# Kernel tuning notes

Measured on AMD Instinct MI355X. Metric: run time of the kernel, lower is better.

The kernel has to match this reference:

```python
import jax, jax.numpy as jnp
import numpy as np
from jax import lax

N_BANDS, TAPS, CUTOFF, BETA = 4, 62, 0.15, 9.0
B, T = 16, 262144


def make_pqmf_filters(N=N_BANDS, taps=TAPS, cutoff=CUTOFF, beta=BETA):
    # scipy.signal.firwin(taps+1, cutoff, window=('kaiser', beta)) reimplemented:
    numtaps = taps + 1
    m = np.arange(numtaps) - (numtaps - 1) / 2.0
    qmf = cutoff * np.sinc(cutoff * m) * np.kaiser(numtaps, beta)
    qmf /= qmf.sum()  # unit DC gain (firwin scale=True, lowpass)
    k = np.arange(N)[:, None]
    n = np.arange(numtaps)[None, :]
    const = (2 * k + 1) * (np.pi / (2 * N)) * (n - (taps - 1) / 2.0)
    phase = ((-1.0) ** np.arange(N))[:, None] * np.pi / 4.0
    H = 2.0 * qmf * np.cos(const + phase)
    G = 2.0 * qmf * np.cos(const - phase)
    return H.astype(np.float32), G.astype(np.float32)


def setup_inputs() -> dict:
    key = jax.random.key(0)
    x = jax.random.normal(key, (B, 1, T), dtype=jnp.float32)
    H, G = make_pqmf_filters()
    return {"x": x, "H": jnp.asarray(H), "G": jnp.asarray(G)}


def reference(x, H, G):
    # Round trip: synthesis(analysis(x)). x: (B,1,T); H,G: (N, taps+1).
    N = H.shape[0]
    pad = (H.shape[1] - 1) // 2  # taps//2 = 31
    dn = ('NCH', 'OIH', 'NCH')
    # analysis: stride-1 FIR bank then the updown_filter strided conv, which is
    # exactly take-every-Nth-sample (updown_filter[0,k,k]=1).
    sub = lax.conv_general_dilated(x, H[:, None, :], (1,), [(pad, pad)],
                                   dimension_numbers=dn)  # (B, N, T)
    sub = sub[:, :, ::N]  # (B, N, T//N)
    # synthesis: conv1d_transpose(updown_filter*N, stride N) == zero-stuff upsample
    # scaled by N; fused here via lhs_dilation. Extra N-1 right pad matches the
    # trailing zeros of the TF transpose-conv output (length T//N * N).
    recon = lax.conv_general_dilated(sub * N, G[None, :, :], (1,),
                                     [(pad, pad + N - 1)], lhs_dilation=(N,),
                                     dimension_numbers=dn)  # (B, 1, T)
    return recon
```

## Files before the change

### kernel.cpp

```cpp
#include <hip/hip_runtime.h>

#define TT 262144
#define BB 16
#define SS 65536
#define QPB 1024
#define TILEQ 1056
#define PX(j) ((j) + ((j) >> 2))
#define LDSQ 1320

__global__ __launch_bounds__(256) void prep_w(const float* __restrict__ H,
                                              const float* __restrict__ G,
                                              float* __restrict__ W) {
    int t = blockIdx.x * 256 + threadIdx.x;
    int e = t >> 2;
    int k = t & 3;
    bool valid = (e < 4 * 132);
    float acc = 0.f;
    if (valid) {
        int p = e / 132;
        int i = e % 132;
        int dd = 126 + p - i;
        if (dd >= 0 && dd <= 124) {
            int j0 = (3 - p) & 3;
#pragma unroll
            for (int jj = 0; jj < 16; ++jj) {
                int j = j0 + 4 * jj;
                if (j <= 62) {
                    int a = 124 - j - dd;
                    if (a >= 0 && a <= 62) acc += H[k * 63 + a] * G[k * 63 + j];
                }
            }
        }
    }
    acc += __shfl_xor(acc, 1);
    acc += __shfl_xor(acc, 2);
    if (valid && k == 0) W[e] = 4.0f * acc;
}

__global__ __launch_bounds__(256) void pqmf_fused(const float* __restrict__ x,
                                                  const float* __restrict__ Wg,
                                                  const float* __restrict__ H,
                                                  const float* __restrict__ G,
                                                  float* __restrict__ out) {
    __shared__ float4 xs4[LDSQ];

    const int tid = threadIdx.x;
    const int b = blockIdx.y;
    const int Q0 = blockIdx.x * QPB;
    const float4* X4 = reinterpret_cast<const float4*>(x + (size_t)b * TT);

    const int gq0 = Q0 - 16;
#pragma unroll
    for (int it = 0; it < 5; ++it) {
        int j = tid + it * 256;
        if (j < TILEQ) {
            int gq = gq0 + j;
            xs4[PX(j)] = (gq >= 0 && gq < SS) ? X4[gq]
                                              : make_float4(0.f, 0.f, 0.f, 0.f);
        }
    }
    __syncthreads();

    const float4* xp = xs4 + 5 * tid;

    float4 a0 = make_float4(0.f, 0.f, 0.f, 0.f);
    float4 a1 = a0, a2 = a0, a3 = a0;

    const float4* W4 = reinterpret_cast<const float4*>(Wg);

#define TAP(k, x0, x1, x2, x3)                                                 \
    {                                                                          \
        const float4 W0 = W4[(k)];                          \
        const float4 W1 = W4[33 + (k)];                     \
        const float4 W2 = W4[66 + (k)];                     \
        const float4 W3 = W4[99 + (k)];                     \
        a0.x = fmaf(W0.w, (x0).w, fmaf(W0.z, (x0).z, fmaf(W0.y, (x0).y, fmaf(W0.x, (x0).x, a0.x)))); \
        a0.y = fmaf(W1.w, (x0).w, fmaf(W1.z, (x0).z, fmaf(W1.y, (x0).y, fmaf(W1.x, (x0).x, a0.y)))); \
        a0.z = fmaf(W2.w, (x0).w, fmaf(W2.z, (x0).z, fmaf(W2.y, (x0).y, fmaf(W2.x, (x0).x, a0.z)))); \
        a0.w = fmaf(W3.w, (x0).w, fmaf(W3.z, (x0).z, fmaf(W3.y, (x0).y, fmaf(W3.x, (x0).x, a0.w)))); \
        a1.x = fmaf(W0.w, (x1).w, fmaf(W0.z, (x1).z, fmaf(W0.y, (x1).y, fmaf(W0.x, (x1).x, a1.x)))); \
        a1.y = fmaf(W1.w, (x1).w, fmaf(W1.z, (x1).z, fmaf(W1.y, (x1).y, fmaf(W1.x, (x1).x, a1.y)))); \
        a1.z = fmaf(W2.w, (x1).w, fmaf(W2.z, (x1).z, fmaf(W2.y, (x1).y, fmaf(W2.x, (x1).x, a1.z)))); \
        a1.w = fmaf(W3.w, (x1).w, fmaf(W3.z, (x1).z, fmaf(W3.y, (x1).y, fmaf(W3.x, (x1).x, a1.w)))); \
        a2.x = fmaf(W0.w, (x2).w, fmaf(W0.z, (x2).z, fmaf(W0.y, (x2).y, fmaf(W0.x, (x2).x, a2.x)))); \
        a2.y = fmaf(W1.w, (x2).w, fmaf(W1.z, (x2).z, fmaf(W1.y, (x2).y, fmaf(W1.x, (x2).x, a2.y)))); \
        a2.z = fmaf(W2.w, (x2).w, fmaf(W2.z, (x2).z, fmaf(W2.y, (x2).y, fmaf(W2.x, (x2).x, a2.z)))); \
        a2.w = fmaf(W3.w, (x2).w, fmaf(W3.z, (x2).z, fmaf(W3.y, (x2).y, fmaf(W3.x, (x2).x, a2.w)))); \
        a3.x = fmaf(W0.w, (x3).w, fmaf(W0.z, (x3).z, fmaf(W0.y, (x3).y, fmaf(W0.x, (x3).x, a3.x)))); \
        a3.y = fmaf(W1.w, (x3).w, fmaf(W1.z, (x3).z, fmaf(W1.y, (x3).y, fmaf(W1.x, (x3).x, a3.y)))); \
        a3.z = fmaf(W2.w, (x3).w, fmaf(W2.z, (x3).z, fmaf(W2.y, (x3).y, fmaf(W2.x, (x3).x, a3.z)))); \
        a3.w = fmaf(W3.w, (x3).w, fmaf(W3.z, (x3).z, fmaf(W3.y, (x3).y, fmaf(W3.x, (x3).x, a3.w)))); \
    }

    float4 w0 = xp[0], w1 = xp[1], w2 = xp[2], w3 = xp[3];

#pragma unroll 1
    for (int mm = 0; mm < 8; ++mm) {
        const float4* xq = xp + 5 * mm;
        const int k0 = 4 * mm;
        float4 n0 = xq[5];
        float4 n1 = xq[6];
        float4 n2 = xq[7];
        float4 n3 = xq[8];
        TAP(k0 + 0, w0, w1, w2, w3)
        TAP(k0 + 1, w1, w2, w3, n0)
        TAP(k0 + 2, w2, w3, n0, n1)
        TAP(k0 + 3, w3, n0, n1, n2)
        w0 = n0; w1 = n1; w2 = n2; w3 = n3;
    }
    TAP(32, w0, w1, w2, w3)
#undef TAP

    float4* ob4 = reinterpret_cast<float4*>(out + (size_t)b * TT);
    const int t0 = tid * 4;
    const int u0 = Q0 + t0;
    if ((unsigned)(u0 - 16) < (unsigned)(SS - 32))     ob4[u0]     = a0;
    if ((unsigned)(u0 + 1 - 16) < (unsigned)(SS - 32)) ob4[u0 + 1] = a1;
    if ((unsigned)(u0 + 2 - 16) < (unsigned)(SS - 32)) ob4[u0 + 2] = a2;
    if ((unsigned)(u0 + 3 - 16) < (unsigned)(SS - 32)) ob4[u0 + 3] = a3;

    const bool edgeLo = (blockIdx.x == 0);
    const bool edgeHi = (blockIdx.x == gridDim.x - 1);
    if (edgeLo || edgeHi) {
        const int q_local = tid >> 4;
        const int s_idx = tid & 15;
        const int u = edgeLo ? q_local : (SS - 16 + q_local);
        const int s = u - 7 + s_idx;
        float c0 = 0.f, c1 = 0.f, c2 = 0.f, c3 = 0.f;
        if (s >= 0 && s < SS) {
            const float* xsf = reinterpret_cast<const float*>(xs4);
            const int lbase = 4 * s - 31 - 4 * Q0 + 64;
            float s0 = 0.f, s1 = 0.f, s2 = 0.f, s3 = 0.f;
#pragma unroll
            for (int a = 0; a < 63; ++a) {
                int ef = lbase + a;
                float xv = xsf[ef + 4 * (ef >> 4)];
                s0 += xv * H[a];
                s1 += xv * H[63 + a];
                s2 += xv * H[126 + a];
                s3 += xv * H[189 + a];
            }
            const int d4 = 4 * (s - u);
            {
                int j = d4 + 31;
                if (j <= 62) c0 = s0 * G[j] + s1 * G[63 + j] + s2 * G[126 + j] + s3 * G[189 + j];
            }
            {
                int j = d4 + 30;
                c1 = s0 * G[j] + s1 * G[63 + j] + s2 * G[126 + j] + s3 * G[189 + j];
            }
            {
                int j = d4 + 29;
                c2 = s0 * G[j] + s1 * G[63 + j] + s2 * G[126 + j] + s3 * G[189 + j];
            }
            {
                int j = d4 + 28;
                c3 = s0 * G[j] + s1 * G[63 + j] + s2 * G[126 + j] + s3 * G[189 + j];
            }
        }
#pragma unroll
        for (int m = 8; m >= 1; m >>= 1) {
            c0 += __shfl_xor(c0, m);
            c1 += __shfl_xor(c1, m);
            c2 += __shfl_xor(c2, m);
            c3 += __shfl_xor(c3, m);
        }
        if (s_idx == 0) {
            float4 v = make_float4(4.f * c0, 4.f * c1, 4.f * c2, 4.f * c3);
            ob4[u] = v;
        }
    }
}

extern "C" void kernel_launch(void* const* d_in, const int* in_sizes, int n_in,
                              void* d_out, int out_size, void* d_ws, size_t ws_size,
                              hipStream_t stream) {
    const float* x = (const float*)d_in[0];
    const float* H = (const float*)d_in[1];
    const float* G = (const float*)d_in[2];
    float* outp = (float*)d_out;
    float* W = (float*)d_ws;

    hipLaunchKernelGGL(prep_w, dim3(9), dim3(256), 0, stream, H, G, W);
    hipLaunchKernelGGL(pqmf_fused, dim3(SS / QPB, BB), dim3(256), 0, stream,
                       x, W, H, G, outp);
}
```

Before: 27.45 us.

## Batch weight loads as 16-wide vectors, unguard interior tile loads, spread edge fixups

Each loop iteration now fetches the weights for four taps as 64-byte vector loads instead of sixteen separate float4 loads. Interior blocks load their input tile with no bounds checks, issuing all global loads before any LDS stores. The 32 edge output quads, previously computed by the two edge blocks with 256 threads, now go one per block to 32 different blocks, using 16 threads that read x straight from global memory. The aim is fewer scalar/vector load instructions on the hot path and less serial tail work in the two edge blocks, at the cost of more registers and a small uncoalesced global read in 32 blocks.

```diff
diff --git a/kernel.cpp b/kernel.cpp
--- a/kernel.cpp
+++ b/kernel.cpp
@@ -7,6 +7,8 @@
 #define TILEQ 1056
 #define PX(j) ((j) + ((j) >> 2))
 #define LDSQ 1320
+
+typedef float floatx16 __attribute__((ext_vector_type(16), aligned(16)));
 
 __global__ __launch_bounds__(256) void prep_w(const float* __restrict__ H,
                                               const float* __restrict__ G,
@@ -45,20 +47,33 @@
     __shared__ float4 xs4[LDSQ];
 
     const int tid = threadIdx.x;
+    const int bx = blockIdx.x;
     const int b = blockIdx.y;
-    const int Q0 = blockIdx.x * QPB;
+    const int Q0 = bx * QPB;
     const float4* X4 = reinterpret_cast<const float4*>(x + (size_t)b * TT);
 
     const int gq0 = Q0 - 16;
-#pragma unroll
-    for (int it = 0; it < 5; ++it) {
-        int j = tid + it * 256;
-        if (j < TILEQ) {
-            int gq = gq0 + j;
-            xs4[PX(j)] = (gq >= 0 && gq < SS) ? X4[gq]
-                                              : make_float4(0.f, 0.f, 0.f, 0.f);
-        }
-    }
+    float4 r0, r1, r2, r3, r4;
+    if (bx > 0 && bx < 63) {
+        r0 = X4[gq0 + tid];
+        r1 = X4[gq0 + tid + 256];
+        r2 = X4[gq0 + tid + 512];
+        r3 = X4[gq0 + tid + 768];
+        if (tid < 32) r4 = X4[gq0 + tid + 1024];
+    } else {
+        const float4 z = make_float4(0.f, 0.f, 0.f, 0.f);
+        int g0 = gq0 + tid, g1 = g0 + 256, g2 = g0 + 512, g3 = g0 + 768, g4 = g0 + 1024;
+        r0 = ((unsigned)g0 < (unsigned)SS) ? X4[g0] : z;
+        r1 = ((unsigned)g1 < (unsigned)SS) ? X4[g1] : z;
+        r2 = ((unsigned)g2 < (unsigned)SS) ? X4[g2] : z;
+        r3 = ((unsigned)g3 < (unsigned)SS) ? X4[g3] : z;
+        if (tid < 32) r4 = ((unsigned)g4 < (unsigned)SS) ? X4[g4] : z;
+    }
+    xs4[PX(tid)]       = r0;
+    xs4[PX(tid + 256)] = r1;
+    xs4[PX(tid + 512)] = r2;
+    xs4[PX(tid + 768)] = r3;
+    if (tid < 32) xs4[PX(tid + 1024)] = r4;
     __syncthreads();
 
     const float4* xp = xs4 + 5 * tid;
@@ -66,50 +81,64 @@
     float4 a0 = make_float4(0.f, 0.f, 0.f, 0.f);
     float4 a1 = a0, a2 = a0, a3 = a0;
 
-    const float4* W4 = reinterpret_cast<const float4*>(Wg);
-
-#define TAP(k, x0, x1, x2, x3)                                                 \
+#define TAPX(d, x0, x1, x2, x3)                                                \
     {                                                                          \
-        const float4 W0 = W4[(k)];                          \
-        const float4 W1 = W4[33 + (k)];                     \
-        const float4 W2 = W4[66 + (k)];                     \
-        const float4 W3 = W4[99 + (k)];                     \
-        a0.x = fmaf(W0.w, (x0).w, fmaf(W0.z, (x0).z, fmaf(W0.y, (x0).y, fmaf(W0.x, (x0).x, a0.x)))); \
-        a0.y = fmaf(W1.w, (x0).w, fmaf(W1.z, (x0).z, fmaf(W1.y, (x0).y, fmaf(W1.x, (x0).x, a0.y)))); \
-        a0.z = fmaf(W2.w, (x0).w, fmaf(W2.z, (x0).z, fmaf(W2.y, (x0).y, fmaf(W2.x, (x0).x, a0.z)))); \
-        a0.w = fmaf(W3.w, (x0).w, fmaf(W3.z, (x0).z, fmaf(W3.y, (x0).y, fmaf(W3.x, (x0).x, a0.w)))); \
-        a1.x = fmaf(W0.w, (x1).w, fmaf(W0.z, (x1).z, fmaf(W0.y, (x1).y, fmaf(W0.x, (x1).x, a1.x)))); \
-        a1.y = fmaf(W1.w, (x1).w, fmaf(W1.z, (x1).z, fmaf(W1.y, (x1).y, fmaf(W1.x, (x1).x, a1.y)))); \
-        a1.z = fmaf(W2.w, (x1).w, fmaf(W2.z, (x1).z, fmaf(W2.y, (x1).y, fmaf(W2.x, (x1).x, a1.z)))); \
-        a1.w = fmaf(W3.w, (x1).w, fmaf(W3.z, (x1).z, fmaf(W3.y, (x1).y, fmaf(W3.x, (x1).x, a1.w)))); \
-        a2.x = fmaf(W0.w, (x2).w, fmaf(W0.z, (x2).z, fmaf(W0.y, (x2).y, fmaf(W0.x, (x2).x, a2.x)))); \
-        a2.y = fmaf(W1.w, (x2).w, fmaf(W1.z, (x2).z, fmaf(W1.y, (x2).y, fmaf(W1.x, (x2).x, a2.y)))); \
-        a2.z = fmaf(W2.w, (x2).w, fmaf(W2.z, (x2).z, fmaf(W2.y, (x2).y, fmaf(W2.x, (x2).x, a2.z)))); \
-        a2.w = fmaf(W3.w, (x2).w, fmaf(W3.z, (x2).z, fmaf(W3.y, (x2).y, fmaf(W3.x, (x2).x, a2.w)))); \
-        a3.x = fmaf(W0.w, (x3).w, fmaf(W0.z, (x3).z, fmaf(W0.y, (x3).y, fmaf(W0.x, (x3).x, a3.x)))); \
-        a3.y = fmaf(W1.w, (x3).w, fmaf(W1.z, (x3).z, fmaf(W1.y, (x3).y, fmaf(W1.x, (x3).x, a3.y)))); \
-        a3.z = fmaf(W2.w, (x3).w, fmaf(W2.z, (x3).z, fmaf(W2.y, (x3).y, fmaf(W2.x, (x3).x, a3.z)))); \
-        a3.w = fmaf(W3.w, (x3).w, fmaf(W3.z, (x3).z, fmaf(W3.y, (x3).y, fmaf(W3.x, (x3).x, a3.w)))); \
+        a0.x = fmaf(P0[4*(d)+3], (x0).w, fmaf(P0[4*(d)+2], (x0).z, fmaf(P0[4*(d)+1], (x0).y, fmaf(P0[4*(d)+0], (x0).x, a0.x)))); \
+        a0.y = fmaf(P1[4*(d)+3], (x0).w, fmaf(P1[4*(d)+2], (x0).z, fmaf(P1[4*(d)+1], (x0).y, fmaf(P1[4*(d)+0], (x0).x, a0.y)))); \
+        a0.z = fmaf(P2[4*(d)+3], (x0).w, fmaf(P2[4*(d)+2], (x0).z, fmaf(P2[4*(d)+1], (x0).y, fmaf(P2[4*(d)+0], (x0).x, a0.z)))); \
+        a0.w = fmaf(P3[4*(d)+3], (x0).w, fmaf(P3[4*(d)+2], (x0).z, fmaf(P3[4*(d)+1], (x0).y, fmaf(P3[4*(d)+0], (x0).x, a0.w)))); \
+        a1.x = fmaf(P0[4*(d)+3], (x1).w, fmaf(P0[4*(d)+2], (x1).z, fmaf(P0[4*(d)+1], (x1).y, fmaf(P0[4*(d)+0], (x1).x, a1.x)))); \
+        a1.y = fmaf(P1[4*(d)+3], (x1).w, fmaf(P1[4*(d)+2], (x1).z, fmaf(P1[4*(d)+1], (x1).y, fmaf(P1[4*(d)+0], (x1).x, a1.y)))); \
+        a1.z = fmaf(P2[4*(d)+3], (x1).w, fmaf(P2[4*(d)+2], (x1).z, fmaf(P2[4*(d)+1], (x1).y, fmaf(P2[4*(d)+0], (x1).x, a1.z)))); \
+        a1.w = fmaf(P3[4*(d)+3], (x1).w, fmaf(P3[4*(d)+2], (x1).z, fmaf(P3[4*(d)+1], (x1).y, fmaf(P3[4*(d)+0], (x1).x, a1.w)))); \
+        a2.x = fmaf(P0[4*(d)+3], (x2).w, fmaf(P0[4*(d)+2], (x2).z, fmaf(P0[4*(d)+1], (x2).y, fmaf(P0[4*(d)+0], (x2).x, a2.x)))); \
+        a2.y = fmaf(P1[4*(d)+3], (x2).w, fmaf(P1[4*(d)+2], (x2).z, fmaf(P1[4*(d)+1], (x2).y, fmaf(P1[4*(d)+0], (x2).x, a2.y)))); \
+        a2.z = fmaf(P2[4*(d)+3], (x2).w, fmaf(P2[4*(d)+2], (x2).z, fmaf(P2[4*(d)+1], (x2).y, fmaf(P2[4*(d)+0], (x2).x, a2.z)))); \
+        a2.w = fmaf(P3[4*(d)+3], (x2).w, fmaf(P3[4*(d)+2], (x2).z, fmaf(P3[4*(d)+1], (x2).y, fmaf(P3[4*(d)+0], (x2).x, a2.w)))); \
+        a3.x = fmaf(P0[4*(d)+3], (x3).w, fmaf(P0[4*(d)+2], (x3).z, fmaf(P0[4*(d)+1], (x3).y, fmaf(P0[4*(d)+0], (x3).x, a3.x)))); \
+        a3.y = fmaf(P1[4*(d)+3], (x3).w, fmaf(P1[4*(d)+2], (x3).z, fmaf(P1[4*(d)+1], (x3).y, fmaf(P1[4*(d)+0], (x3).x, a3.y)))); \
+        a3.z = fmaf(P2[4*(d)+3], (x3).w, fmaf(P2[4*(d)+2], (x3).z, fmaf(P2[4*(d)+1], (x3).y, fmaf(P2[4*(d)+0], (x3).x, a3.z)))); \
+        a3.w = fmaf(P3[4*(d)+3], (x3).w, fmaf(P3[4*(d)+2], (x3).z, fmaf(P3[4*(d)+1], (x3).y, fmaf(P3[4*(d)+0], (x3).x, a3.w)))); \
     }
 
     float4 w0 = xp[0], w1 = xp[1], w2 = xp[2], w3 = xp[3];
 
 #pragma unroll 1
     for (int mm = 0; mm < 8; ++mm) {
+        const int k0 = 4 * mm;
+        const floatx16 P0 = *reinterpret_cast<const floatx16*>(Wg + 4 * k0);
+        const floatx16 P1 = *reinterpret_cast<const floatx16*>(Wg + 132 + 4 * k0);
+        const floatx16 P2 = *reinterpret_cast<const floatx16*>(Wg + 264 + 4 * k0);
+        const floatx16 P3 = *reinterpret_cast<const floatx16*>(Wg + 396 + 4 * k0);
         const float4* xq = xp + 5 * mm;
-        const int k0 = 4 * mm;
         float4 n0 = xq[5];
         float4 n1 = xq[6];
         float4 n2 = xq[7];
         float4 n3 = xq[8];
-        TAP(k0 + 0, w0, w1, w2, w3)
-        TAP(k0 + 1, w1, w2, w3, n0)
-        TAP(k0 + 2, w2, w3, n0, n1)
-        TAP(k0 + 3, w3, n0, n1, n2)
+        TAPX(0, w0, w1, w2, w3)
+        TAPX(1, w1, w2, w3, n0)
+        TAPX(2, w2, w3, n0, n1)
+        TAPX(3, w3, n0, n1, n2)
         w0 = n0; w1 = n1; w2 = n2; w3 = n3;
     }
-    TAP(32, w0, w1, w2, w3)
-#undef TAP
+#undef TAPX
+
+    {
+        const float4 T0 = *reinterpret_cast<const float4*>(Wg + 128);
+        const float4 T1 = *reinterpret_cast<const float4*>(Wg + 132 + 128);
+        const float4 T2 = *reinterpret_cast<const float4*>(Wg + 264 + 128);
+        const float4 T3 = *reinterpret_cast<const float4*>(Wg + 396 + 128);
+#define TT4(ar, xv)                                                            \
+        ar.x = fmaf(T0.w, (xv).w, fmaf(T0.z, (xv).z, fmaf(T0.y, (xv).y, fmaf(T0.x, (xv).x, ar.x)))); \
+        ar.y = fmaf(T1.w, (xv).w, fmaf(T1.z, (xv).z, fmaf(T1.y, (xv).y, fmaf(T1.x, (xv).x, ar.y)))); \
+        ar.z = fmaf(T2.w, (xv).w, fmaf(T2.z, (xv).z, fmaf(T2.y, (xv).y, fmaf(T2.x, (xv).x, ar.z)))); \
+        ar.w = fmaf(T3.w, (xv).w, fmaf(T3.z, (xv).z, fmaf(T3.y, (xv).y, fmaf(T3.x, (xv).x, ar.w))));
+        TT4(a0, w0)
+        TT4(a1, w1)
+        TT4(a2, w2)
+        TT4(a3, w3)
+#undef TT4
+    }
 
     float4* ob4 = reinterpret_cast<float4*>(out + (size_t)b * TT);
     const int t0 = tid * 4;
@@ -119,28 +148,26 @@
     if ((unsigned)(u0 + 2 - 16) < (unsigned)(SS - 32)) ob4[u0 + 2] = a2;
     if ((unsigned)(u0 + 3 - 16) < (unsigned)(SS - 32)) ob4[u0 + 3] = a3;
 
-    const bool edgeLo = (blockIdx.x == 0);
-    const bool edgeHi = (blockIdx.x == gridDim.x - 1);
-    if (edgeLo || edgeHi) {
-        const int q_local = tid >> 4;
-        const int s_idx = tid & 15;
-        const int u = edgeLo ? q_local : (SS - 16 + q_local);
-        const int s = u - 7 + s_idx;
+    int ue = -1;
+    if (bx < 16) ue = bx;
+    else if (bx >= 48) ue = SS - 64 + bx;
+    if (ue >= 0 && tid < 16) {
+        const float* xb = x + (size_t)b * TT;
+        const int s = ue - 7 + tid;
         float c0 = 0.f, c1 = 0.f, c2 = 0.f, c3 = 0.f;
         if (s >= 0 && s < SS) {
-            const float* xsf = reinterpret_cast<const float*>(xs4);
-            const int lbase = 4 * s - 31 - 4 * Q0 + 64;
+            const int xbase = 4 * s - 31;
             float s0 = 0.f, s1 = 0.f, s2 = 0.f, s3 = 0.f;
 #pragma unroll
             for (int a = 0; a < 63; ++a) {
-                int ef = lbase + a;
-                float xv = xsf[ef + 4 * (ef >> 4)];
+                int xi = xbase + a;
+                float xv = (xi >= 0 && xi < TT) ? xb[xi] : 0.f;
                 s0 += xv * H[a];
                 s1 += xv * H[63 + a];
                 s2 += xv * H[126 + a];
                 s3 += xv * H[189 + a];
             }
-            const int d4 = 4 * (s - u);
+            const int d4 = 4 * (s - ue);
             {
                 int j = d4 + 31;
                 if (j <= 62) c0 = s0 * G[j] + s1 * G[63 + j] + s2 * G[126 + j] + s3 * G[189 + j];
@@ -165,9 +192,9 @@
             c2 += __shfl_xor(c2, m);
             c3 += __shfl_xor(c3, m);
         }
-        if (s_idx == 0) {
+        if (tid == 0) {
             float4 v = make_float4(4.f * c0, 4.f * c1, 4.f * c2, 4.f * c3);
-            ob4[u] = v;
+            ob4[ue] = v;
         }
     }
 }
```

New measurement: 34.25 us. +24.8%, slower.

## Process two half-size tiles per block with register-prefetched second tile

Applied to the files above, without the earlier changes.

Blocks shrink to 128 threads and 512 quads per tile, and each block now handles two tiles (bx and bx+64). The second tile's global loads go into registers before the first tile is computed, then get stored to a second LDS buffer. The aim is to hide global load latency behind compute. The grid drops to 64x16 blocks of 128 threads, which lowers parallelism and occupancy across the device. Edge handling is split into two passes of 8 outputs to fit the smaller block.

```diff
diff --git a/kernel.cpp b/kernel.cpp
--- a/kernel.cpp
+++ b/kernel.cpp
@@ -3,10 +3,11 @@
 #define TT 262144
 #define BB 16
 #define SS 65536
-#define QPB 1024
-#define TILEQ 1056
+#define QPB 512
+#define TILEQ 544
+#define NTHR 128
 #define PX(j) ((j) + ((j) >> 2))
-#define LDSQ 1320
+#define LDSQ 680
 
 __global__ __launch_bounds__(256) void prep_w(const float* __restrict__ H,
                                               const float* __restrict__ G,
@@ -36,37 +37,6 @@
     acc += __shfl_xor(acc, 2);
     if (valid && k == 0) W[e] = 4.0f * acc;
 }
-
-__global__ __launch_bounds__(256) void pqmf_fused(const float* __restrict__ x,
-                                                  const float* __restrict__ Wg,
-                                                  const float* __restrict__ H,
-                                                  const float* __restrict__ G,
-                                                  float* __restrict__ out) {
-    __shared__ float4 xs4[LDSQ];
-
-    const int tid = threadIdx.x;
-    const int b = blockIdx.y;
-    const int Q0 = blockIdx.x * QPB;
-    const float4* X4 = reinterpret_cast<const float4*>(x + (size_t)b * TT);
-
-    const int gq0 = Q0 - 16;
-#pragma unroll
-    for (int it = 0; it < 5; ++it) {
-        int j = tid + it * 256;
-        if (j < TILEQ) {
-            int gq = gq0 + j;
-            xs4[PX(j)] = (gq >= 0 && gq < SS) ? X4[gq]
-                                              : make_float4(0.f, 0.f, 0.f, 0.f);
-        }
-    }
-    __syncthreads();
-
-    const float4* xp = xs4 + 5 * tid;
-
-    float4 a0 = make_float4(0.f, 0.f, 0.f, 0.f);
-    float4 a1 = a0, a2 = a0, a3 = a0;
-
-    const float4* W4 = reinterpret_cast<const float4*>(Wg);
 
 #define TAP(k, x0, x1, x2, x3)                                                 \
     {                                                                          \
@@ -92,8 +62,15 @@
         a3.w = fmaf(W3.w, (x3).w, fmaf(W3.z, (x3).z, fmaf(W3.y, (x3).y, fmaf(W3.x, (x3).x, a3.w)))); \
     }
 
+__device__ __forceinline__ void compute_tile(const float4* __restrict__ xsb,
+                                             const float4* __restrict__ W4,
+                                             float4* __restrict__ ob4,
+                                             int Q0, int tid) {
+    const float4* xp = xsb + 5 * tid;
+    float4 a0 = make_float4(0.f, 0.f, 0.f, 0.f);
+    float4 a1 = a0, a2 = a0, a3 = a0;
+
     float4 w0 = xp[0], w1 = xp[1], w2 = xp[2], w3 = xp[3];
-
 #pragma unroll 1
     for (int mm = 0; mm < 8; ++mm) {
         const float4* xq = xp + 5 * mm;
@@ -109,26 +86,27 @@
         w0 = n0; w1 = n1; w2 = n2; w3 = n3;
     }
     TAP(32, w0, w1, w2, w3)
-#undef TAP
-
-    float4* ob4 = reinterpret_cast<float4*>(out + (size_t)b * TT);
-    const int t0 = tid * 4;
-    const int u0 = Q0 + t0;
+
+    const int u0 = Q0 + 4 * tid;
     if ((unsigned)(u0 - 16) < (unsigned)(SS - 32))     ob4[u0]     = a0;
     if ((unsigned)(u0 + 1 - 16) < (unsigned)(SS - 32)) ob4[u0 + 1] = a1;
     if ((unsigned)(u0 + 2 - 16) < (unsigned)(SS - 32)) ob4[u0 + 2] = a2;
     if ((unsigned)(u0 + 3 - 16) < (unsigned)(SS - 32)) ob4[u0 + 3] = a3;
-
-    const bool edgeLo = (blockIdx.x == 0);
-    const bool edgeHi = (blockIdx.x == gridDim.x - 1);
-    if (edgeLo || edgeHi) {
-        const int q_local = tid >> 4;
+}
+
+__device__ __forceinline__ void edge16(const float* __restrict__ xsf, int Q0,
+                                       const float* __restrict__ H,
+                                       const float* __restrict__ G,
+                                       float4* __restrict__ ob4,
+                                       int uBase, int tid) {
+#pragma unroll 1
+    for (int half = 0; half < 2; ++half) {
+        const int q_local = (tid >> 4) + 8 * half;
         const int s_idx = tid & 15;
-        const int u = edgeLo ? q_local : (SS - 16 + q_local);
+        const int u = uBase + q_local;
         const int s = u - 7 + s_idx;
         float c0 = 0.f, c1 = 0.f, c2 = 0.f, c3 = 0.f;
         if (s >= 0 && s < SS) {
-            const float* xsf = reinterpret_cast<const float*>(xs4);
             const int lbase = 4 * s - 31 - 4 * Q0 + 64;
             float s0 = 0.f, s1 = 0.f, s2 = 0.f, s3 = 0.f;
 #pragma unroll
@@ -170,6 +148,65 @@
             ob4[u] = v;
         }
     }
+}
+
+__global__ __launch_bounds__(NTHR) void pqmf_fused(const float* __restrict__ x,
+                                                   const float* __restrict__ Wg,
+                                                   const float* __restrict__ H,
+                                                   const float* __restrict__ G,
+                                                   float* __restrict__ out) {
+    __shared__ float4 xs4[2][LDSQ];
+
+    const int tid = threadIdx.x;
+    const int bx = blockIdx.x;
+    const int b = blockIdx.y;
+    const int Q0a = bx * QPB;
+    const int Q0b = (bx + 64) * QPB;
+    const float4* X4 = reinterpret_cast<const float4*>(x + (size_t)b * TT);
+    const float4* W4 = reinterpret_cast<const float4*>(Wg);
+    float4* ob4 = reinterpret_cast<float4*>(out + (size_t)b * TT);
+    const float4 z = make_float4(0.f, 0.f, 0.f, 0.f);
+
+    {
+        const int gq0 = Q0a - 16;
+#pragma unroll
+        for (int it = 0; it < 5; ++it) {
+            int j = tid + it * NTHR;
+            if (j < TILEQ) {
+                int gq = gq0 + j;
+                xs4[0][PX(j)] = ((unsigned)gq < (unsigned)SS) ? X4[gq] : z;
+            }
+        }
+    }
+    __syncthreads();
+
+    const int gq0b = Q0b - 16;
+    float4 r0, r1, r2, r3, r4;
+    {
+        int g0 = gq0b + tid;
+        int g1 = g0 + NTHR, g2 = g0 + 2 * NTHR, g3 = g0 + 3 * NTHR, g4 = g0 + 4 * NTHR;
+        r0 = ((unsigned)g0 < (unsigned)SS) ? X4[g0] : z;
+        r1 = ((unsigned)g1 < (unsigned)SS) ? X4[g1] : z;
+        r2 = ((unsigned)g2 < (unsigned)SS) ? X4[g2] : z;
+        r3 = ((unsigned)g3 < (unsigned)SS) ? X4[g3] : z;
+        r4 = (tid < TILEQ - 4 * NTHR && (unsigned)g4 < (unsigned)SS) ? X4[g4] : z;
+    }
+
+    compute_tile(xs4[0], W4, ob4, Q0a, tid);
+
+    xs4[1][PX(tid)]            = r0;
+    xs4[1][PX(tid + NTHR)]     = r1;
+    xs4[1][PX(tid + 2 * NTHR)] = r2;
+    xs4[1][PX(tid + 3 * NTHR)] = r3;
+    if (tid < TILEQ - 4 * NTHR) xs4[1][PX(tid + 4 * NTHR)] = r4;
+    __syncthreads();
+
+    compute_tile(xs4[1], W4, ob4, Q0b, tid);
+
+    if (bx == 0)
+        edge16(reinterpret_cast<const float*>(xs4[0]), Q0a, H, G, ob4, 0, tid);
+    if (bx == 63)
+        edge16(reinterpret_cast<const float*>(xs4[1]), Q0b, H, G, ob4, SS - 16, tid);
 }
 
 extern "C" void kernel_launch(void* const* d_in, const int* in_sizes, int n_in,
@@ -182,6 +219,6 @@
     float* W = (float*)d_ws;
 
     hipLaunchKernelGGL(prep_w, dim3(9), dim3(256), 0, stream, H, G, W);
-    hipLaunchKernelGGL(pqmf_fused, dim3(SS / QPB, BB), dim3(256), 0, stream,
+    hipLaunchKernelGGL(pqmf_fused, dim3(64, BB), dim3(NTHR), 0, stream,
                        x, W, H, G, outp);
 }
```

Measured after the change: 31.19 us. +13.6%, slower.
